# Performance work log

Hardware: AMD Instinct MI355X
Metric: run time of the kernel (lower is better)

Reference implementation:

```python
import jax, jax.numpy as jnp
import numpy as np

N = 100000        # num nodes
F_IN = 256        # params['topo_feature']
C = 128           # params['num_edge'] (hidden & GCN channels)
E = 1_600_000     # num edges (avg degree 16)


def setup_inputs() -> dict:
    key = jax.random.key(0)
    k = jax.random.split(key, 6)
    x = jax.random.normal(k[0], (N, F_IN), dtype=jnp.float32)
    edge_index = jax.random.randint(k[1], (2, E), 0, N, dtype=jnp.int32)
    # fc1: Linear(F_IN, C)
    W1 = jax.random.normal(k[2], (C, F_IN), dtype=jnp.float32) * (1.0 / np.sqrt(F_IN))
    b1 = jnp.zeros((C,), dtype=jnp.float32)
    # GCNConv linear: Linear(C, C, bias=False) weight + separate bias added post-aggregation
    W2 = jax.random.normal(k[3], (C, C), dtype=jnp.float32) * (1.0 / np.sqrt(C))
    b2 = jnp.zeros((C,), dtype=jnp.float32)
    return {"x": x, "edge_index": edge_index, "W1": W1, "b1": b1, "W2": W2, "b2": b2}


def reference(x, edge_index, W1, b1, W2, b2):
    # fc1 + relu
    h = jax.nn.relu(x @ W1.T + b1)                       # [N, C]
    # GCNConv: transform, add self-loops, sym-normalize, scatter-add
    z = h @ W2.T                                         # [N, C]
    loop = jnp.arange(N, dtype=edge_index.dtype)
    src = jnp.concatenate([edge_index[0], loop])         # [E+N]
    dst = jnp.concatenate([edge_index[1], loop])         # [E+N]
    deg = jax.ops.segment_sum(jnp.ones_like(dst, jnp.float32), dst, num_segments=N)
    dinv = jnp.where(deg > 0, jax.lax.rsqrt(jnp.maximum(deg, 1.0)), 0.0)
    norm = (dinv[src] * dinv[dst])[:, None]              # [E+N, 1]
    out = jax.ops.segment_sum(z[src] * norm, dst, num_segments=N) + b2
    return out
```

## Files before the change

### kernel.cpp

```cpp
#include <hip/hip_runtime.h>

typedef unsigned short ushort;
typedef __bf16 bf16x8 __attribute__((ext_vector_type(8)));
typedef float f32x4 __attribute__((ext_vector_type(4)));

#define F_IN 256
#define CCH  128
#define BSH  7
#define BNODES 128
#define NBUCK 1024
#define CHUNK 2048

__device__ __forceinline__ ushort f2bf(float f) {
    union { float f; unsigned i; } u; u.f = f;
    unsigned r = u.i + 0x7fffu + ((u.i >> 16) & 1u);
    return (ushort)(r >> 16);
}
__device__ __forceinline__ float2 bf2f2(unsigned u) {
    union { unsigned i; float f; } lo, hi;
    lo.i = u << 16;
    hi.i = u & 0xffff0000u;
    return make_float2(lo.f, hi.f);
}
__device__ __forceinline__ void gload_lds16(const void* g, void* l) {
    __builtin_amdgcn_global_load_lds((const __attribute__((address_space(1))) unsigned*)g,
                                     (__attribute__((address_space(3))) unsigned*)l, 16, 0, 0);
}

__global__ __launch_bounds__(256)
void hist_cvt(const int* __restrict__ dst, int* __restrict__ histC, int* __restrict__ histT,
              int E, int nchunks, int ncp,
              const float* __restrict__ W1, const float* __restrict__ W2,
              ushort* __restrict__ w1b, ushort* __restrict__ w2b)
{
    const int blk = blockIdx.x, t = threadIdx.x;
    if (blk >= nchunks) {
        int i = (blk - nchunks) * 256 + t;
        if (i < CCH * F_IN) {
            int c  = i & 31;
            int cs = c ^ (((i >> 9) & 3) << 3);
            w1b[(i & ~31) | cs] = f2bf(W1[i]);
        } else {
            int j = i - CCH * F_IN;
            if (j < CCH * CCH) w2b[j] = f2bf(W2[j]);
        }
        return;
    }
    __shared__ int h[NBUCK];
    for (int i = t; i < NBUCK; i += 256) h[i] = 0;
    __syncthreads();
    int cb = blk * CHUNK, ce = min(cb + CHUNK, E);
    for (int e = cb + t; e < ce; e += 256)
        atomicAdd(&h[dst[e] >> BSH], 1);
    __syncthreads();
    for (int i = t; i < NBUCK; i += 256) {
        int v = h[i];
        histC[blk * NBUCK + i] = v;
        histT[i * ncp + blk]   = v;
    }
}

__global__ __launch_bounds__(256)
void scan_buckets(const int* __restrict__ histT, int* __restrict__ prefT,
                  int* __restrict__ btot, int nchunks, int ncp)
{
    const int b = blockIdx.x * 4 + (threadIdx.x >> 6);
    const int lane = threadIdx.x & 63;
    int carry = 0;
    for (int c = 0; c < nchunks; c += 64) {
        int idx = c + lane;
        int v = (idx < nchunks) ? histT[b * ncp + idx] : 0;
        int inc = v;
#pragma unroll
        for (int off = 1; off < 64; off <<= 1) {
            int x = __shfl_up(inc, off, 64);
            if (lane >= off) inc += x;
        }
        if (idx < nchunks) prefT[b * ncp + idx] = carry + inc - v;
        carry += __shfl(inc, 63, 64);
    }
    if (lane == 0) btot[b] = carry;
}

__global__ __launch_bounds__(256)
void partition_kernel(const int* __restrict__ src, const int* __restrict__ dst,
                      const int* __restrict__ histC, const int* __restrict__ prefT,
                      const int* __restrict__ btot, int* __restrict__ gbase,
                      unsigned* __restrict__ pairs, int E, int ncp)
{
    __shared__ int lbase[NBUCK];
    __shared__ int lcur[NBUCK];
    __shared__ int rb2[NBUCK];
    __shared__ int base_s[NBUCK];
    __shared__ int ssum[256];
    __shared__ unsigned sp[CHUNK];
    __shared__ ushort  sb[CHUNK];
    const int t = threadIdx.x, blk = blockIdx.x;

    int4 cv = *(const int4*)&histC[blk * NBUCK + 4 * t];
    int tsum = cv.x + cv.y + cv.z + cv.w;
    ssum[t] = tsum;
    __syncthreads();
    for (int off = 1; off < 256; off <<= 1) {
        int x = (t >= off) ? ssum[t - off] : 0;
        __syncthreads();
        ssum[t] += x;
        __syncthreads();
    }
    int texcl = ssum[t] - tsum;
    lbase[4 * t]     = texcl;
    lbase[4 * t + 1] = texcl + cv.x;
    lbase[4 * t + 2] = texcl + cv.x + cv.y;
    lbase[4 * t + 3] = texcl + cv.x + cv.y + cv.z;
    lcur[4 * t]     = lbase[4 * t];
    lcur[4 * t + 1] = lbase[4 * t + 1];
    lcur[4 * t + 2] = lbase[4 * t + 2];
    lcur[4 * t + 3] = lbase[4 * t + 3];
    __syncthreads();

    int4 bt = *(const int4*)&btot[4 * t];
    int bsum = bt.x + bt.y + bt.z + bt.w;
    ssum[t] = bsum;
    __syncthreads();
    for (int off = 1; off < 256; off <<= 1) {
        int x = (t >= off) ? ssum[t - off] : 0;
        __syncthreads();
        ssum[t] += x;
        __syncthreads();
    }
    int bexcl = ssum[t] - bsum;
    base_s[4 * t]     = bexcl;
    base_s[4 * t + 1] = bexcl + bt.x;
    base_s[4 * t + 2] = bexcl + bt.x + bt.y;
    base_s[4 * t + 3] = bexcl + bt.x + bt.y + bt.z;
    if (blk == 0) {
        *(int4*)&gbase[4 * t] = *(int4*)&base_s[4 * t];
        if (t == 255) gbase[NBUCK] = ssum[255];
    }
    __syncthreads();
    for (int i = t; i < NBUCK; i += 256)
        rb2[i] = base_s[i] + prefT[i * ncp + blk];
    __syncthreads();

    const int cb = blk * CHUNK, ce = min(cb + CHUNK, E);
    for (int e = cb + t; e < ce; e += 256) {
        int d = dst[e];
        int b = d >> BSH;
        unsigned packed = ((unsigned)src[e] << BSH) | (unsigned)(d & (BNODES - 1));
        int p = atomicAdd(&lcur[b], 1);
        sp[p] = packed;
        sb[p] = (ushort)b;
    }
    __syncthreads();
    const int cnt = ce - cb;
    for (int i = t; i < cnt; i += 256) {
        int b = sb[i];
        pairs[rb2[b] + (i - lbase[b])] = sp[i];
    }
}

__global__ __launch_bounds__(256)
void bucket_csr(const unsigned* __restrict__ pairs, const int* __restrict__ base,
                int* __restrict__ row_start, float* __restrict__ dinv,
                unsigned* __restrict__ csr, int N, int E)
{
    __shared__ int deg[BNODES];
    __shared__ int s[BNODES];
    __shared__ int cur[BNODES];
    const int b = blockIdx.x, t = threadIdx.x;
    if (t < BNODES) deg[t] = 0;
    __syncthreads();
    const int rb = base[b], re = base[b + 1];
    for (int e = rb + t; e < re; e += 256)
        atomicAdd(&deg[pairs[e] & (BNODES - 1)], 1);
    __syncthreads();
    int v = (t < BNODES) ? deg[t] : 0;
    if (t < BNODES) s[t] = v;
    __syncthreads();
    for (int off = 1; off < BNODES; off <<= 1) {
        int x = (t >= off && t < BNODES) ? s[t - off] : 0;
        __syncthreads();
        if (t < BNODES) s[t] += x;
        __syncthreads();
    }
    const int n0 = b << BSH;
    if (t < BNODES) {
        int excl = s[t] - v;
        cur[t] = excl;
        if (n0 + t < N) {
            row_start[n0 + t] = rb + excl;
            dinv[n0 + t] = rsqrtf((float)v + 1.0f);
        }
    }
    if (b == gridDim.x - 1 && t == 0) row_start[N] = E;
    __syncthreads();
    for (int e = rb + t; e < re; e += 256) {
        unsigned p = pairs[e];
        int l = p & (BNODES - 1);
        int slot = atomicAdd(&cur[l], 1);
        csr[rb + slot] = p >> BSH;
    }
}

__global__ __launch_bounds__(256)
void gemm_fused(const float* __restrict__ X, const ushort* __restrict__ W1b,
                const ushort* __restrict__ W2b, const float* __restrict__ b1,
                const float* __restrict__ dinv, ushort* __restrict__ Zq, int M)
{
    __shared__ ushort smem[16384];
    ushort* Ht = smem;
    const int tid  = threadIdx.x;
    const int wave = tid >> 6, lane = tid & 63;
    const int wm = (wave & 1) * 64, wn = (wave >> 1) * 64;
    const int lr = lane & 15, lq = lane >> 4;
    const int m0 = blockIdx.x * 128;

    const int arow = tid >> 2;
    const int aq   = tid & 3;

    float4 ar[2][2];
    auto loadX = [&](int k0) {
#pragma unroll
        for (int it = 0; it < 2; it++) {
            int row = arow + it * 64;
            ar[it][0] = make_float4(0.f, 0.f, 0.f, 0.f);
            ar[it][1] = make_float4(0.f, 0.f, 0.f, 0.f);
            if (m0 + row < M) {
                const float* p = &X[(long)(m0 + row) * F_IN + k0 + aq * 8];
                ar[it][0] = *(const float4*)p;
                ar[it][1] = *(const float4*)(p + 4);
            }
        }
    };
    auto writeA = [&](ushort* As) {
#pragma unroll
        for (int it = 0; it < 2; it++) {
            int row = arow + it * 64;
            ushort u[8] = { f2bf(ar[it][0].x), f2bf(ar[it][0].y), f2bf(ar[it][0].z), f2bf(ar[it][0].w),
                            f2bf(ar[it][1].x), f2bf(ar[it][1].y), f2bf(ar[it][1].z), f2bf(ar[it][1].w) };
            *(uint4*)&As[row * 32 + ((aq ^ ((row >> 1) & 3)) << 3)] = *(uint4*)u;
        }
    };
    auto stageB = [&](int k0, ushort* Bs) {
#pragma unroll
        for (int it = 0; it < 2; it++) {
            int r0 = wave * 32 + it * 16;
            const ushort* g = &W1b[(long)(r0 + (lane >> 2)) * F_IN + k0 + (lane & 3) * 8];
            gload_lds16(g, &Bs[r0 * 32]);
        }
    };

    f32x4 acc[4][4] = {};
    loadX(0);
    stageB(0, smem + 4096);
    writeA(smem);
    __syncthreads();
    for (int k0 = 0; k0 < F_IN; k0 += 32) {
        const int cur = (k0 >> 5) & 1;
        ushort* As = smem + cur * 8192;
        ushort* Bs = As + 4096;
        const bool more = (k0 + 32 < F_IN);
        if (more) {
            stageB(k0 + 32, smem + (cur ^ 1) * 8192 + 4096);
            loadX(k0 + 32);
        }
        bf16x8 af[4], bfr[4];
#pragma unroll
        for (int t4 = 0; t4 < 4; t4++) {
            int ra = wm + t4 * 16 + lr;
            int rb = wn + t4 * 16 + lr;
            af[t4]  = *(bf16x8*)&As[ra * 32 + ((lq ^ ((ra >> 1) & 3)) << 3)];
            bfr[t4] = *(bf16x8*)&Bs[rb * 32 + ((lq ^ ((rb >> 1) & 3)) << 3)];
        }
#pragma unroll
        for (int i = 0; i < 4; i++)
#pragma unroll
            for (int j = 0; j < 4; j++)
                acc[i][j] = __builtin_amdgcn_mfma_f32_16x16x32_bf16(af[i], bfr[j], acc[i][j], 0, 0, 0);
        if (more) writeA(smem + (cur ^ 1) * 8192);
        __syncthreads();
    }

    uint4 wb[2][4];
#pragma unroll
    for (int t4 = 0; t4 < 4; t4++)
        wb[0][t4] = *(const uint4*)&W2b[(long)(wn + t4 * 16 + lr) * CCH + lq * 8];

    {
        float bv[4];
#pragma unroll
        for (int j = 0; j < 4; j++) bv[j] = b1[wn + j * 16 + lr];
#pragma unroll
        for (int i = 0; i < 4; i++)
#pragma unroll
            for (int r = 0; r < 4; r++) {
                int row = wm + i * 16 + lq * 4 + r;
                int rx  = (row & 7) << 3;
#pragma unroll
                for (int j = 0; j < 4; j++)
                    Ht[row * 128 + ((wn + j * 16 + lr) ^ rx)] = f2bf(fmaxf(acc[i][j][r] + bv[j], 0.f));
            }
    }
    __syncthreads();

    f32x4 acc2[4][4] = {};
#pragma unroll
    for (int kk = 0; kk < 4; kk++) {
        const int k0 = kk * 32;
        if (kk < 3) {
#pragma unroll
            for (int t4 = 0; t4 < 4; t4++)
                wb[(kk + 1) & 1][t4] =
                    *(const uint4*)&W2b[(long)(wn + t4 * 16 + lr) * CCH + k0 + 32 + lq * 8];
        }
        bf16x8 af[4];
#pragma unroll
        for (int t4 = 0; t4 < 4; t4++) {
            int ra = wm + t4 * 16 + lr;
            af[t4] = *(bf16x8*)&Ht[ra * 128 + ((k0 + lq * 8) ^ ((ra & 7) << 3))];
        }
#pragma unroll
        for (int i = 0; i < 4; i++)
#pragma unroll
            for (int j = 0; j < 4; j++)
                acc2[i][j] = __builtin_amdgcn_mfma_f32_16x16x32_bf16(af[i], *(bf16x8*)&wb[kk & 1][j],
                                                                     acc2[i][j], 0, 0, 0);
    }
    __syncthreads();

#pragma unroll
    for (int i = 0; i < 4; i++)
#pragma unroll
        for (int r = 0; r < 4; r++) {
            int row = wm + i * 16 + lq * 4 + r;
            int rx  = (row & 7) << 3;
            float di = (m0 + row < M) ? dinv[m0 + row] : 0.f;
#pragma unroll
            for (int j = 0; j < 4; j++)
                Ht[row * 128 + ((wn + j * 16 + lr) ^ rx)] = f2bf(acc2[i][j][r] * di);
        }
    __syncthreads();
    {
        int colq = tid & 15, row0 = tid >> 4;
#pragma unroll
        for (int i = 0; i < 8; i++) {
            int row = row0 + i * 16;
            if (m0 + row < M)
                *(uint4*)&Zq[(long)(m0 + row) * CCH + colq * 8] =
                    *(uint4*)&Ht[row * 128 + ((colq * 8) ^ ((row & 7) << 3))];
        }
    }
}

__global__ __launch_bounds__(256)
void gather_nodes(const unsigned* __restrict__ zq, const unsigned* __restrict__ csr,
                  const int* __restrict__ row_start, const float* __restrict__ dinv,
                  const float* __restrict__ b2, float* __restrict__ out, int N)
{
    const int node = blockIdx.x * 4 + (threadIdx.x >> 6);
    const int lane = threadIdx.x & 63;
    if (node >= N) return;

    float2 zs = bf2f2(zq[(long)node * 64 + lane]);
    float acc0 = zs.x, acc1 = zs.y;

    const int rs = row_start[node];
    const int re = row_start[node + 1];
    int j = rs;
    for (; j + 8 <= re; j += 8) {
        unsigned sI[8], zv[8];
#pragma unroll
        for (int q = 0; q < 8; q++) sI[q] = csr[j + q];
#pragma unroll
        for (int q = 0; q < 8; q++) zv[q] = zq[(long)sI[q] * 64 + lane];
#pragma unroll
        for (int q = 0; q < 8; q++) { float2 f = bf2f2(zv[q]); acc0 += f.x; acc1 += f.y; }
    }
    for (; j < re; j++) {
        float2 f = bf2f2(zq[(long)csr[j] * 64 + lane]);
        acc0 += f.x; acc1 += f.y;
    }

    float di = dinv[node];
    float2 o;
    o.x = b2[lane * 2 + 0] + di * acc0;
    o.y = b2[lane * 2 + 1] + di * acc1;
    *(float2*)&out[(long)node * CCH + lane * 2] = o;
}

extern "C" void kernel_launch(void* const* d_in, const int* in_sizes, int n_in,
                              void* d_out, int out_size, void* d_ws, size_t ws_size,
                              hipStream_t stream)
{
    const float* x  = (const float*)d_in[0];
    const int*   ei = (const int*)d_in[1];
    const float* W1 = (const float*)d_in[2];
    const float* b1 = (const float*)d_in[3];
    const float* W2 = (const float*)d_in[4];
    const float* b2 = (const float*)d_in[5];
    float* out = (float*)d_out;

    const int N = in_sizes[0] / F_IN;
    const int E = in_sizes[1] / 2;
    const int* src = ei;
    const int* dst = ei + E;

    const int nchunks = (E + CHUNK - 1) / CHUNK;
    const int ncp     = (nchunks + 63) & ~63;
    const int nbuck   = (N + BNODES - 1) / BNODES;
    const int ngrid   = (N + 127) / 128;
    const int ncvt    = (CCH * F_IN + CCH * CCH + 255) / 256;

    char* ws = (char*)d_ws;
    ushort* zq    = (ushort*)ws;   ws += (size_t)N * CCH * 2;
    ushort* w1b   = (ushort*)ws;   ws += (size_t)CCH * F_IN * 2;
    ushort* w2b   = (ushort*)ws;   ws += (size_t)CCH * CCH * 2;
    unsigned* prs = (unsigned*)ws; ws += (size_t)E * 4;
    unsigned* csr = (unsigned*)ws; ws += (size_t)E * 4;
    int* rstart   = (int*)ws;      ws += ((size_t)N + 1) * 4;
    float* dinv   = (float*)ws;    ws += (size_t)N * 4;
    int* histC    = (int*)ws;      ws += (size_t)nchunks * NBUCK * 4;
    int* histT    = (int*)ws;      ws += (size_t)NBUCK * ncp * 4;
    int* prefT    = (int*)ws;      ws += (size_t)NBUCK * ncp * 4;
    int* btot     = (int*)ws;      ws += NBUCK * 4;
    int* gbase    = (int*)ws;      ws += (NBUCK + 1) * 4;

    hist_cvt<<<nchunks + ncvt, 256, 0, stream>>>(dst, histC, histT, E, nchunks, ncp, W1, W2, w1b, w2b);
    scan_buckets<<<NBUCK / 4, 256, 0, stream>>>(histT, prefT, btot, nchunks, ncp);
    partition_kernel<<<nchunks, 256, 0, stream>>>(src, dst, histC, prefT, btot, gbase, prs, E, ncp);
    bucket_csr<<<nbuck, 256, 0, stream>>>(prs, gbase, rstart, dinv, csr, N, E);

    gemm_fused<<<ngrid, 256, 0, stream>>>(x, w1b, w2b, b1, dinv, zq, N);

    gather_nodes<<<(N + 3) / 4, 256, 0, stream>>>((const unsigned*)zq, csr, rstart, dinv, b2, out, N);
}
```

Baseline: 323.1 us.

## Co-schedule GEMM halves with partition and CSR build; move source dinv scaling to gather

The source-side dinv scaling moves out of the GEMM epilogue and into the gather kernel, which now loads dinv per neighbor. That removes the GEMM's dependency on the degree computation. The GEMM is then split in half, and each half is merged as a block range into the partition and CSR-building kernels, so the compute-bound GEMM blocks run alongside the memory-bound graph preprocessing. The cost is an extra random dinv load per edge in the gather, plus larger shared memory in the merged kernels, which can lower occupancy for the partition and CSR blocks.

```diff
diff --git a/kernel.cpp b/kernel.cpp
--- a/kernel.cpp
+++ b/kernel.cpp
@@ -82,20 +82,20 @@
     if (lane == 0) btot[b] = carry;
 }
 
-__global__ __launch_bounds__(256)
-void partition_kernel(const int* __restrict__ src, const int* __restrict__ dst,
-                      const int* __restrict__ histC, const int* __restrict__ prefT,
-                      const int* __restrict__ btot, int* __restrict__ gbase,
-                      unsigned* __restrict__ pairs, int E, int ncp)
-{
-    __shared__ int lbase[NBUCK];
-    __shared__ int lcur[NBUCK];
-    __shared__ int rb2[NBUCK];
-    __shared__ int base_s[NBUCK];
-    __shared__ int ssum[256];
-    __shared__ unsigned sp[CHUNK];
-    __shared__ ushort  sb[CHUNK];
-    const int t = threadIdx.x, blk = blockIdx.x;
+__device__ __forceinline__ void partition_body(unsigned* smem4,
+    const int* __restrict__ src, const int* __restrict__ dst,
+    const int* __restrict__ histC, const int* __restrict__ prefT,
+    const int* __restrict__ btot, int* __restrict__ gbase,
+    unsigned* __restrict__ pairs, int E, int ncp, int blk)
+{
+    int* lbase  = (int*)smem4;
+    int* lcur   = lbase + NBUCK;
+    int* rb2    = lcur + NBUCK;
+    int* base_s = rb2 + NBUCK;
+    int* ssum   = base_s + NBUCK;
+    unsigned* sp = (unsigned*)(ssum + 256);
+    ushort* sb  = (ushort*)(sp + CHUNK);
+    const int t = threadIdx.x;
 
     int4 cv = *(const int4*)&histC[blk * NBUCK + 4 * t];
     int tsum = cv.x + cv.y + cv.z + cv.w;
@@ -159,15 +159,15 @@
     }
 }
 
-__global__ __launch_bounds__(256)
-void bucket_csr(const unsigned* __restrict__ pairs, const int* __restrict__ base,
-                int* __restrict__ row_start, float* __restrict__ dinv,
-                unsigned* __restrict__ csr, int N, int E)
-{
-    __shared__ int deg[BNODES];
-    __shared__ int s[BNODES];
-    __shared__ int cur[BNODES];
-    const int b = blockIdx.x, t = threadIdx.x;
+__device__ __forceinline__ void csr_body(unsigned* smem4,
+    const unsigned* __restrict__ pairs, const int* __restrict__ base,
+    int* __restrict__ row_start, float* __restrict__ dinv,
+    unsigned* __restrict__ csr, int N, int E, int b, int lastb)
+{
+    int* deg = (int*)smem4;
+    int* s   = deg + BNODES;
+    int* cur = s + BNODES;
+    const int t = threadIdx.x;
     if (t < BNODES) deg[t] = 0;
     __syncthreads();
     const int rb = base[b], re = base[b + 1];
@@ -192,7 +192,7 @@
             dinv[n0 + t] = rsqrtf((float)v + 1.0f);
         }
     }
-    if (b == gridDim.x - 1 && t == 0) row_start[N] = E;
+    if (b == lastb && t == 0) row_start[N] = E;
     __syncthreads();
     for (int e = rb + t; e < re; e += 256) {
         unsigned p = pairs[e];
@@ -202,18 +202,17 @@
     }
 }
 
-__global__ __launch_bounds__(256)
-void gemm_fused(const float* __restrict__ X, const ushort* __restrict__ W1b,
-                const ushort* __restrict__ W2b, const float* __restrict__ b1,
-                const float* __restrict__ dinv, ushort* __restrict__ Zq, int M)
-{
-    __shared__ ushort smem[16384];
+__device__ __forceinline__ void gemm_body(unsigned* smem4,
+    const float* __restrict__ X, const ushort* __restrict__ W1b,
+    const ushort* __restrict__ W2b, const float* __restrict__ b1,
+    ushort* __restrict__ Zq, int M, int m0)
+{
+    ushort* smem = (ushort*)smem4;
     ushort* Ht = smem;
     const int tid  = threadIdx.x;
     const int wave = tid >> 6, lane = tid & 63;
     const int wm = (wave & 1) * 64, wn = (wave >> 1) * 64;
     const int lr = lane & 15, lq = lane >> 4;
-    const int m0 = blockIdx.x * 128;
 
     const int arow = tid >> 2;
     const int aq   = tid & 3;
@@ -334,10 +333,9 @@
         for (int r = 0; r < 4; r++) {
             int row = wm + i * 16 + lq * 4 + r;
             int rx  = (row & 7) << 3;
-            float di = (m0 + row < M) ? dinv[m0 + row] : 0.f;
 #pragma unroll
             for (int j = 0; j < 4; j++)
-                Ht[row * 128 + ((wn + j * 16 + lr) ^ rx)] = f2bf(acc2[i][j][r] * di);
+                Ht[row * 128 + ((wn + j * 16 + lr) ^ rx)] = f2bf(acc2[i][j][r]);
         }
     __syncthreads();
     {
@@ -353,6 +351,39 @@
 }
 
 __global__ __launch_bounds__(256)
+void u_part_gemm(const int* __restrict__ src, const int* __restrict__ dst,
+                 const int* __restrict__ histC, const int* __restrict__ prefT,
+                 const int* __restrict__ btot, int* __restrict__ gbase,
+                 unsigned* __restrict__ pairs, int E, int ncp, int ngA,
+                 const float* __restrict__ X, const ushort* __restrict__ W1b,
+                 const ushort* __restrict__ W2b, const float* __restrict__ b1,
+                 ushort* __restrict__ Zq, int M)
+{
+    __shared__ unsigned smem4[8192];
+    if ((int)blockIdx.x < ngA)
+        gemm_body(smem4, X, W1b, W2b, b1, Zq, M, blockIdx.x * 128);
+    else
+        partition_body(smem4, src, dst, histC, prefT, btot, gbase, pairs, E, ncp,
+                       blockIdx.x - ngA);
+}
+
+__global__ __launch_bounds__(256)
+void u_csr_gemm(const unsigned* __restrict__ pairs, const int* __restrict__ base,
+                int* __restrict__ row_start, float* __restrict__ dinv,
+                unsigned* __restrict__ csr, int N, int E, int ngB, int ngA, int nbuck,
+                const float* __restrict__ X, const ushort* __restrict__ W1b,
+                const ushort* __restrict__ W2b, const float* __restrict__ b1,
+                ushort* __restrict__ Zq, int M)
+{
+    __shared__ unsigned smem4[8192];
+    if ((int)blockIdx.x < ngB)
+        gemm_body(smem4, X, W1b, W2b, b1, Zq, M, (ngA + blockIdx.x) * 128);
+    else
+        csr_body(smem4, pairs, base, row_start, dinv, csr, N, E,
+                 blockIdx.x - ngB, nbuck - 1);
+}
+
+__global__ __launch_bounds__(256)
 void gather_nodes(const unsigned* __restrict__ zq, const unsigned* __restrict__ csr,
                   const int* __restrict__ row_start, const float* __restrict__ dinv,
                   const float* __restrict__ b2, float* __restrict__ out, int N)
@@ -361,27 +392,32 @@
     const int lane = threadIdx.x & 63;
     if (node >= N) return;
 
+    const float di = dinv[node];
     float2 zs = bf2f2(zq[(long)node * 64 + lane]);
-    float acc0 = zs.x, acc1 = zs.y;
+    float acc0 = di * zs.x, acc1 = di * zs.y;
 
     const int rs = row_start[node];
     const int re = row_start[node + 1];
     int j = rs;
     for (; j + 8 <= re; j += 8) {
         unsigned sI[8], zv[8];
+        float dv[8];
 #pragma unroll
         for (int q = 0; q < 8; q++) sI[q] = csr[j + q];
 #pragma unroll
+        for (int q = 0; q < 8; q++) dv[q] = dinv[sI[q]];
+#pragma unroll
         for (int q = 0; q < 8; q++) zv[q] = zq[(long)sI[q] * 64 + lane];
 #pragma unroll
-        for (int q = 0; q < 8; q++) { float2 f = bf2f2(zv[q]); acc0 += f.x; acc1 += f.y; }
+        for (int q = 0; q < 8; q++) { float2 f = bf2f2(zv[q]); acc0 += dv[q] * f.x; acc1 += dv[q] * f.y; }
     }
     for (; j < re; j++) {
-        float2 f = bf2f2(zq[(long)csr[j] * 64 + lane]);
-        acc0 += f.x; acc1 += f.y;
-    }
-
-    float di = dinv[node];
+        unsigned s = csr[j];
+        float ds = dinv[s];
+        float2 f = bf2f2(zq[(long)s * 64 + lane]);
+        acc0 += ds * f.x; acc1 += ds * f.y;
+    }
+
     float2 o;
     o.x = b2[lane * 2 + 0] + di * acc0;
     o.y = b2[lane * 2 + 1] + di * acc1;
@@ -409,6 +445,8 @@
     const int ncp     = (nchunks + 63) & ~63;
     const int nbuck   = (N + BNODES - 1) / BNODES;
     const int ngrid   = (N + 127) / 128;
+    const int ngA     = (ngrid + 1) / 2;
+    const int ngB     = ngrid - ngA;
     const int ncvt    = (CCH * F_IN + CCH * CCH + 255) / 256;
 
     char* ws = (char*)d_ws;
@@ -427,10 +465,9 @@
 
     hist_cvt<<<nchunks + ncvt, 256, 0, stream>>>(dst, histC, histT, E, nchunks, ncp, W1, W2, w1b, w2b);
     scan_buckets<<<NBUCK / 4, 256, 0, stream>>>(histT, prefT, btot, nchunks, ncp);
-    partition_kernel<<<nchunks, 256, 0, stream>>>(src, dst, histC, prefT, btot, gbase, prs, E, ncp);
-    bucket_csr<<<nbuck, 256, 0, stream>>>(prs, gbase, rstart, dinv, csr, N, E);
-
-    gemm_fused<<<ngrid, 256, 0, stream>>>(x, w1b, w2b, b1, dinv, zq, N);
-
+    u_part_gemm<<<ngA + nchunks, 256, 0, stream>>>(src, dst, histC, prefT, btot, gbase, prs, E, ncp,
+                                                   ngA, x, w1b, w2b, b1, zq, N);
+    u_csr_gemm<<<ngB + nbuck, 256, 0, stream>>>(prs, gbase, rstart, dinv, csr, N, E,
+                                                ngB, ngA, nbuck, x, w1b, w2b, b1, zq, N);
     gather_nodes<<<(N + 3) / 4, 256, 0, stream>>>((const unsigned*)zq, csr, rstart, dinv, b2, out, N);
 }
```

Result: no change. 318.8 us (-1.3%).

## Replace bucket-sort CSR build with atomic degree count, scan, and scatter

Applied to the files above, without the earlier changes.

Drops the multi-pass histogram, partition and bucket CSR build. Degrees are now counted with global atomics inside the GEMM kernel, then a three-kernel prefix scan runs, then edges are scattered into CSR with per-node atomic cursors. Because the GEMM no longer depends on dinv, the source-side normalization moves into the gather kernel through an extra dinv[src] load per edge. The change removes passes over the edge list, but it adds heavy global atomic contention, a nondeterministic CSR order, and extra random loads in the gather.

```diff
diff --git a/kernel.cpp b/kernel.cpp
--- a/kernel.cpp
+++ b/kernel.cpp
@@ -6,10 +6,6 @@
 
 #define F_IN 256
 #define CCH  128
-#define BSH  7
-#define BNODES 128
-#define NBUCK 1024
-#define CHUNK 2048
 
 __device__ __forceinline__ ushort f2bf(float f) {
     union { float f; unsigned i; } u; u.f = f;
@@ -28,14 +24,13 @@
 }
 
 __global__ __launch_bounds__(256)
-void hist_cvt(const int* __restrict__ dst, int* __restrict__ histC, int* __restrict__ histT,
-              int E, int nchunks, int ncp,
-              const float* __restrict__ W1, const float* __restrict__ W2,
-              ushort* __restrict__ w1b, ushort* __restrict__ w2b)
+void cvt_zero(const float* __restrict__ W1, const float* __restrict__ W2,
+              ushort* __restrict__ w1b, ushort* __restrict__ w2b,
+              int* __restrict__ deg, int N, int ncvt)
 {
     const int blk = blockIdx.x, t = threadIdx.x;
-    if (blk >= nchunks) {
-        int i = (blk - nchunks) * 256 + t;
+    if (blk < ncvt) {
+        int i = blk * 256 + t;
         if (i < CCH * F_IN) {
             int c  = i & 31;
             int cs = c ^ (((i >> 9) & 3) << 3);
@@ -46,174 +41,22 @@
         }
         return;
     }
-    __shared__ int h[NBUCK];
-    for (int i = t; i < NBUCK; i += 256) h[i] = 0;
-    __syncthreads();
-    int cb = blk * CHUNK, ce = min(cb + CHUNK, E);
-    for (int e = cb + t; e < ce; e += 256)
-        atomicAdd(&h[dst[e] >> BSH], 1);
-    __syncthreads();
-    for (int i = t; i < NBUCK; i += 256) {
-        int v = h[i];
-        histC[blk * NBUCK + i] = v;
-        histT[i * ncp + blk]   = v;
-    }
-}
-
-__global__ __launch_bounds__(256)
-void scan_buckets(const int* __restrict__ histT, int* __restrict__ prefT,
-                  int* __restrict__ btot, int nchunks, int ncp)
-{
-    const int b = blockIdx.x * 4 + (threadIdx.x >> 6);
-    const int lane = threadIdx.x & 63;
-    int carry = 0;
-    for (int c = 0; c < nchunks; c += 64) {
-        int idx = c + lane;
-        int v = (idx < nchunks) ? histT[b * ncp + idx] : 0;
-        int inc = v;
-#pragma unroll
-        for (int off = 1; off < 64; off <<= 1) {
-            int x = __shfl_up(inc, off, 64);
-            if (lane >= off) inc += x;
-        }
-        if (idx < nchunks) prefT[b * ncp + idx] = carry + inc - v;
-        carry += __shfl(inc, 63, 64);
-    }
-    if (lane == 0) btot[b] = carry;
-}
-
-__global__ __launch_bounds__(256)
-void partition_kernel(const int* __restrict__ src, const int* __restrict__ dst,
-                      const int* __restrict__ histC, const int* __restrict__ prefT,
-                      const int* __restrict__ btot, int* __restrict__ gbase,
-                      unsigned* __restrict__ pairs, int E, int ncp)
-{
-    __shared__ int lbase[NBUCK];
-    __shared__ int lcur[NBUCK];
-    __shared__ int rb2[NBUCK];
-    __shared__ int base_s[NBUCK];
-    __shared__ int ssum[256];
-    __shared__ unsigned sp[CHUNK];
-    __shared__ ushort  sb[CHUNK];
-    const int t = threadIdx.x, blk = blockIdx.x;
-
-    int4 cv = *(const int4*)&histC[blk * NBUCK + 4 * t];
-    int tsum = cv.x + cv.y + cv.z + cv.w;
-    ssum[t] = tsum;
-    __syncthreads();
-    for (int off = 1; off < 256; off <<= 1) {
-        int x = (t >= off) ? ssum[t - off] : 0;
-        __syncthreads();
-        ssum[t] += x;
-        __syncthreads();
-    }
-    int texcl = ssum[t] - tsum;
-    lbase[4 * t]     = texcl;
-    lbase[4 * t + 1] = texcl + cv.x;
-    lbase[4 * t + 2] = texcl + cv.x + cv.y;
-    lbase[4 * t + 3] = texcl + cv.x + cv.y + cv.z;
-    lcur[4 * t]     = lbase[4 * t];
-    lcur[4 * t + 1] = lbase[4 * t + 1];
-    lcur[4 * t + 2] = lbase[4 * t + 2];
-    lcur[4 * t + 3] = lbase[4 * t + 3];
-    __syncthreads();
-
-    int4 bt = *(const int4*)&btot[4 * t];
-    int bsum = bt.x + bt.y + bt.z + bt.w;
-    ssum[t] = bsum;
-    __syncthreads();
-    for (int off = 1; off < 256; off <<= 1) {
-        int x = (t >= off) ? ssum[t - off] : 0;
-        __syncthreads();
-        ssum[t] += x;
-        __syncthreads();
-    }
-    int bexcl = ssum[t] - bsum;
-    base_s[4 * t]     = bexcl;
-    base_s[4 * t + 1] = bexcl + bt.x;
-    base_s[4 * t + 2] = bexcl + bt.x + bt.y;
-    base_s[4 * t + 3] = bexcl + bt.x + bt.y + bt.z;
-    if (blk == 0) {
-        *(int4*)&gbase[4 * t] = *(int4*)&base_s[4 * t];
-        if (t == 255) gbase[NBUCK] = ssum[255];
-    }
-    __syncthreads();
-    for (int i = t; i < NBUCK; i += 256)
-        rb2[i] = base_s[i] + prefT[i * ncp + blk];
-    __syncthreads();
-
-    const int cb = blk * CHUNK, ce = min(cb + CHUNK, E);
-    for (int e = cb + t; e < ce; e += 256) {
-        int d = dst[e];
-        int b = d >> BSH;
-        unsigned packed = ((unsigned)src[e] << BSH) | (unsigned)(d & (BNODES - 1));
-        int p = atomicAdd(&lcur[b], 1);
-        sp[p] = packed;
-        sb[p] = (ushort)b;
-    }
-    __syncthreads();
-    const int cnt = ce - cb;
-    for (int i = t; i < cnt; i += 256) {
-        int b = sb[i];
-        pairs[rb2[b] + (i - lbase[b])] = sp[i];
-    }
-}
-
-__global__ __launch_bounds__(256)
-void bucket_csr(const unsigned* __restrict__ pairs, const int* __restrict__ base,
-                int* __restrict__ row_start, float* __restrict__ dinv,
-                unsigned* __restrict__ csr, int N, int E)
-{
-    __shared__ int deg[BNODES];
-    __shared__ int s[BNODES];
-    __shared__ int cur[BNODES];
-    const int b = blockIdx.x, t = threadIdx.x;
-    if (t < BNODES) deg[t] = 0;
-    __syncthreads();
-    const int rb = base[b], re = base[b + 1];
-    for (int e = rb + t; e < re; e += 256)
-        atomicAdd(&deg[pairs[e] & (BNODES - 1)], 1);
-    __syncthreads();
-    int v = (t < BNODES) ? deg[t] : 0;
-    if (t < BNODES) s[t] = v;
-    __syncthreads();
-    for (int off = 1; off < BNODES; off <<= 1) {
-        int x = (t >= off && t < BNODES) ? s[t - off] : 0;
-        __syncthreads();
-        if (t < BNODES) s[t] += x;
-        __syncthreads();
-    }
-    const int n0 = b << BSH;
-    if (t < BNODES) {
-        int excl = s[t] - v;
-        cur[t] = excl;
-        if (n0 + t < N) {
-            row_start[n0 + t] = rb + excl;
-            dinv[n0 + t] = rsqrtf((float)v + 1.0f);
-        }
-    }
-    if (b == gridDim.x - 1 && t == 0) row_start[N] = E;
-    __syncthreads();
-    for (int e = rb + t; e < re; e += 256) {
-        unsigned p = pairs[e];
-        int l = p & (BNODES - 1);
-        int slot = atomicAdd(&cur[l], 1);
-        csr[rb + slot] = p >> BSH;
-    }
-}
-
-__global__ __launch_bounds__(256)
-void gemm_fused(const float* __restrict__ X, const ushort* __restrict__ W1b,
-                const ushort* __restrict__ W2b, const float* __restrict__ b1,
-                const float* __restrict__ dinv, ushort* __restrict__ Zq, int M)
-{
-    __shared__ ushort smem[16384];
+    int i = (blk - ncvt) * 1024 + t * 4;
+    if (i + 3 < N) *(int4*)&deg[i] = make_int4(0, 0, 0, 0);
+    else { for (int q = 0; q < 4; q++) if (i + q < N) deg[i + q] = 0; }
+}
+
+__device__ __forceinline__ void gemm_body(unsigned* smem4,
+    const float* __restrict__ X, const ushort* __restrict__ W1b,
+    const ushort* __restrict__ W2b, const float* __restrict__ b1,
+    ushort* __restrict__ Zq, int M, int m0)
+{
+    ushort* smem = (ushort*)smem4;
     ushort* Ht = smem;
     const int tid  = threadIdx.x;
     const int wave = tid >> 6, lane = tid & 63;
     const int wm = (wave & 1) * 64, wn = (wave >> 1) * 64;
     const int lr = lane & 15, lq = lane >> 4;
-    const int m0 = blockIdx.x * 128;
 
     const int arow = tid >> 2;
     const int aq   = tid & 3;
@@ -334,10 +177,9 @@
         for (int r = 0; r < 4; r++) {
             int row = wm + i * 16 + lq * 4 + r;
             int rx  = (row & 7) << 3;
-            float di = (m0 + row < M) ? dinv[m0 + row] : 0.f;
 #pragma unroll
             for (int j = 0; j < 4; j++)
-                Ht[row * 128 + ((wn + j * 16 + lr) ^ rx)] = f2bf(acc2[i][j][r] * di);
+                Ht[row * 128 + ((wn + j * 16 + lr) ^ rx)] = f2bf(acc2[i][j][r]);
         }
     __syncthreads();
     {
@@ -353,7 +195,117 @@
 }
 
 __global__ __launch_bounds__(256)
-void gather_nodes(const unsigned* __restrict__ zq, const unsigned* __restrict__ csr,
+void gemm_count(const float* __restrict__ X, const ushort* __restrict__ W1b,
+                const ushort* __restrict__ W2b, const float* __restrict__ b1,
+                ushort* __restrict__ Zq, int M,
+                const int* __restrict__ dst, int* __restrict__ deg, int E, int eper)
+{
+    __shared__ unsigned smem4[8192];
+    gemm_body(smem4, X, W1b, W2b, b1, Zq, M, blockIdx.x * 128);
+    const int e0 = blockIdx.x * eper;
+    const int e1 = min(e0 + eper, E);
+    for (int e = e0 + (int)threadIdx.x; e < e1; e += 256)
+        atomicAdd(&deg[dst[e]], 1);
+}
+
+__global__ __launch_bounds__(256)
+void scan_sums(const int* __restrict__ deg, int* __restrict__ bsum, int N)
+{
+    __shared__ int s[256];
+    const int t = threadIdx.x;
+    int base = blockIdx.x * 1024 + t * 4;
+    int v = 0;
+    if (base + 3 < N) { int4 d = *(const int4*)&deg[base]; v = d.x + d.y + d.z + d.w; }
+    else { for (int q = 0; q < 4; q++) if (base + q < N) v += deg[base + q]; }
+    s[t] = v;
+    __syncthreads();
+    for (int off = 128; off > 0; off >>= 1) {
+        if (t < off) s[t] += s[t + off];
+        __syncthreads();
+    }
+    if (t == 0) bsum[blockIdx.x] = s[0];
+}
+
+__global__ __launch_bounds__(128)
+void scan_top(const int* __restrict__ bsum, int* __restrict__ boff, int nb)
+{
+    __shared__ int s[128];
+    const int t = threadIdx.x;
+    int carry = 0;
+    for (int c = 0; c < nb; c += 128) {
+        int idx = c + t;
+        int v = (idx < nb) ? bsum[idx] : 0;
+        s[t] = v;
+        __syncthreads();
+        for (int off = 1; off < 128; off <<= 1) {
+            int x = (t >= off) ? s[t - off] : 0;
+            __syncthreads();
+            s[t] += x;
+            __syncthreads();
+        }
+        if (idx < nb) boff[idx] = carry + s[t] - v;
+        carry += s[127];
+        __syncthreads();
+    }
+}
+
+__global__ __launch_bounds__(256)
+void scan_final(const int* __restrict__ deg, const int* __restrict__ boff,
+                int* __restrict__ rstart, int* __restrict__ cur,
+                float* __restrict__ dinv, int N, int E)
+{
+    __shared__ int s[256];
+    const int t = threadIdx.x;
+    int base = blockIdx.x * 1024 + t * 4;
+    int4 d = make_int4(0, 0, 0, 0);
+    if (base + 3 < N) d = *(const int4*)&deg[base];
+    else {
+        if (base + 0 < N) d.x = deg[base + 0];
+        if (base + 1 < N) d.y = deg[base + 1];
+        if (base + 2 < N) d.z = deg[base + 2];
+    }
+    int tsum = d.x + d.y + d.z + d.w;
+    s[t] = tsum;
+    __syncthreads();
+    for (int off = 1; off < 256; off <<= 1) {
+        int x = (t >= off) ? s[t - off] : 0;
+        __syncthreads();
+        s[t] += x;
+        __syncthreads();
+    }
+    int excl = boff[blockIdx.x] + s[t] - tsum;
+    int r0 = excl, r1 = r0 + d.x, r2 = r1 + d.y, r3 = r2 + d.z;
+    if (base + 3 < N) {
+        *(int4*)&rstart[base]  = make_int4(r0, r1, r2, r3);
+        *(int4*)&cur[base]     = make_int4(r0, r1, r2, r3);
+        *(float4*)&dinv[base]  = make_float4(rsqrtf((float)d.x + 1.f), rsqrtf((float)d.y + 1.f),
+                                             rsqrtf((float)d.z + 1.f), rsqrtf((float)d.w + 1.f));
+    } else {
+        int rr[4] = { r0, r1, r2, r3 };
+        int dd[4] = { d.x, d.y, d.z, d.w };
+        for (int q = 0; q < 4; q++) if (base + q < N) {
+            rstart[base + q] = rr[q];
+            cur[base + q]    = rr[q];
+            dinv[base + q]   = rsqrtf((float)dd[q] + 1.f);
+        }
+    }
+    if (blockIdx.x == 0 && t == 0) rstart[N] = E;
+}
+
+__global__ __launch_bounds__(256)
+void scatter(const int* __restrict__ src, const int* __restrict__ dst,
+             int* __restrict__ cur, int* __restrict__ csr, int E)
+{
+    const int stride = gridDim.x * 256;
+    for (int e = blockIdx.x * 256 + threadIdx.x; e < E; e += stride) {
+        int d = dst[e];
+        int slot = atomicAdd(&cur[d], 1);
+        csr[slot] = src[e];
+    }
+}
+
+__global__ __launch_bounds__(256)
+void gather_nodes(const unsigned* __restrict__ zq, const int* __restrict__ csr,
                   const int* __restrict__ row_start, const float* __restrict__ dinv,
                   const float* __restrict__ b2, float* __restrict__ out, int N)
 {
@@ -361,27 +313,31 @@
     const int lane = threadIdx.x & 63;
     if (node >= N) return;
 
+    const float di = dinv[node];
     float2 zs = bf2f2(zq[(long)node * 64 + lane]);
-    float acc0 = zs.x, acc1 = zs.y;
+    float acc0 = di * zs.x, acc1 = di * zs.y;
 
     const int rs = row_start[node];
     const int re = row_start[node + 1];
     int j = rs;
     for (; j + 8 <= re; j += 8) {
-        unsigned sI[8], zv[8];
+        int sI[8]; unsigned zv[8]; float dv[8];
 #pragma unroll
         for (int q = 0; q < 8; q++) sI[q] = csr[j + q];
 #pragma unroll
+        for (int q = 0; q < 8; q++) dv[q] = dinv[sI[q]];
+#pragma unroll
         for (int q = 0; q < 8; q++) zv[q] = zq[(long)sI[q] * 64 + lane];
 #pragma unroll
-        for (int q = 0; q < 8; q++) { float2 f = bf2f2(zv[q]); acc0 += f.x; acc1 += f.y; }
+        for (int q = 0; q < 8; q++) { float2 f = bf2f2(zv[q]); acc0 += dv[q] * f.x; acc1 += dv[q] * f.y; }
     }
     for (; j < re; j++) {
-        float2 f = bf2f2(zq[(long)csr[j] * 64 + lane]);
-        acc0 += f.x; acc1 += f.y;
-    }
-
-    float di = dinv[node];
+        int sidx = csr[j];
+        float ds = dinv[sidx];
+        float2 f = bf2f2(zq[(long)sidx * 64 + lane]);
+        acc0 += ds * f.x; acc1 += ds * f.y;
+    }
+
     float2 o;
     o.x = b2[lane * 2 + 0] + di * acc0;
     o.y = b2[lane * 2 + 1] + di * acc1;
@@ -405,32 +361,28 @@
     const int* src = ei;
     const int* dst = ei + E;
 
-    const int nchunks = (E + CHUNK - 1) / CHUNK;
-    const int ncp     = (nchunks + 63) & ~63;
-    const int nbuck   = (N + BNODES - 1) / BNODES;
-    const int ngrid   = (N + 127) / 128;
-    const int ncvt    = (CCH * F_IN + CCH * CCH + 255) / 256;
+    const int ngrid = (N + 127) / 128;
+    const int ncvt  = (CCH * F_IN + CCH * CCH + 255) / 256;
+    const int nz    = (N + 1023) / 1024;
+    const int eper  = (E + ngrid - 1) / ngrid;
 
     char* ws = (char*)d_ws;
-    ushort* zq    = (ushort*)ws;   ws += (size_t)N * CCH * 2;
-    ushort* w1b   = (ushort*)ws;   ws += (size_t)CCH * F_IN * 2;
-    ushort* w2b   = (ushort*)ws;   ws += (size_t)CCH * CCH * 2;
-    unsigned* prs = (unsigned*)ws; ws += (size_t)E * 4;
-    unsigned* csr = (unsigned*)ws; ws += (size_t)E * 4;
-    int* rstart   = (int*)ws;      ws += ((size_t)N + 1) * 4;
-    float* dinv   = (float*)ws;    ws += (size_t)N * 4;
-    int* histC    = (int*)ws;      ws += (size_t)nchunks * NBUCK * 4;
-    int* histT    = (int*)ws;      ws += (size_t)NBUCK * ncp * 4;
-    int* prefT    = (int*)ws;      ws += (size_t)NBUCK * ncp * 4;
-    int* btot     = (int*)ws;      ws += NBUCK * 4;
-    int* gbase    = (int*)ws;      ws += (NBUCK + 1) * 4;
-
-    hist_cvt<<<nchunks + ncvt, 256, 0, stream>>>(dst, histC, histT, E, nchunks, ncp, W1, W2, w1b, w2b);
-    scan_buckets<<<NBUCK / 4, 256, 0, stream>>>(histT, prefT, btot, nchunks, ncp);
-    partition_kernel<<<nchunks, 256, 0, stream>>>(src, dst, histC, prefT, btot, gbase, prs, E, ncp);
-    bucket_csr<<<nbuck, 256, 0, stream>>>(prs, gbase, rstart, dinv, csr, N, E);
-
-    gemm_fused<<<ngrid, 256, 0, stream>>>(x, w1b, w2b, b1, dinv, zq, N);
-
+    ushort* zq  = (ushort*)ws; ws += (size_t)N * CCH * 2;
+    ushort* w1b = (ushort*)ws; ws += (size_t)CCH * F_IN * 2;
+    ushort* w2b = (ushort*)ws; ws += (size_t)CCH * CCH * 2;
+    int* csr    = (int*)ws;    ws += (size_t)E * 4;
+    int* deg    = (int*)ws;    ws += (size_t)N * 4;
+    int* cur    = (int*)ws;    ws += (size_t)N * 4;
+    float* dinv = (float*)ws;  ws += (size_t)N * 4;
+    int* rstart = (int*)ws;    ws += ((size_t)N + 1) * 4;
+    int* bsum   = (int*)ws;    ws += (size_t)nz * 4;
+    int* boff   = (int*)ws;    ws += (size_t)nz * 4;
+
+    cvt_zero<<<ncvt + nz, 256, 0, stream>>>(W1, W2, w1b, w2b, deg, N, ncvt);
+    gemm_count<<<ngrid, 256, 0, stream>>>(x, w1b, w2b, b1, zq, N, dst, deg, E, eper);
+    scan_sums<<<nz, 256, 0, stream>>>(deg, bsum, N);
+    scan_top<<<1, 128, 0, stream>>>(bsum, boff, nz);
+    scan_final<<<nz, 256, 0, stream>>>(deg, boff, rstart, cur, dinv, N, E);
+    scatter<<<1024, 256, 0, stream>>>(src, dst, cur, csr, E);
     gather_nodes<<<(N + 3) / 4, 256, 0, stream>>>((const unsigned*)zq, csr, rstart, dinv, b2, out, N);
 }
```

After: 458.1 us. 41.8% more time.
